# Kernel tuning notes

Hardware: AMD Instinct MI355X
Metric: run time of the kernel (lower is better)

## Reference

```python
import jax, jax.numpy as jnp
import numpy as np

B, H, S, D = 2, 12, 2048, 128
SCALE = D ** (-0.5)
LAMBDA_INIT = 0.8


def setup_inputs() -> dict:
    key = jax.random.key(0)
    ks = jax.random.split(key, 5)
    shp = (B, H, S, D)
    return {
        "q1": jax.random.normal(ks[0], shp, dtype=jnp.float32),
        "k1": jax.random.normal(ks[1], shp, dtype=jnp.float32),
        "v": jax.random.normal(ks[2], shp, dtype=jnp.float32),
        "q2": jax.random.normal(ks[3], shp, dtype=jnp.float32),
        "k2": jax.random.normal(ks[4], shp, dtype=jnp.float32),
        # learnable lambda parameter, stored in log space (lambda_init=0.8)
        "lambda_log": jnp.full((1,), np.log(LAMBDA_INIT), dtype=jnp.float32),
    }


def _causal_attn(q, k, v, causal_mask):
    # q,k,v: [B,H,S,D]; causal_mask: [S,S] bool (True = keep)
    scores = jnp.einsum("bhqd,bhkd->bhqk", q, k) * SCALE
    neg = jnp.asarray(jnp.finfo(scores.dtype).min, scores.dtype)
    scores = jnp.where(causal_mask, scores, neg)
    weights = jax.nn.softmax(scores, axis=-1)
    return jnp.einsum("bhqk,bhkd->bhqd", weights, v)


def reference(q1, k1, v, q2, k2, lambda_log):
    seq = q1.shape[2]
    causal_mask = jnp.tril(jnp.ones((seq, seq), dtype=bool))
    attn1 = _causal_attn(q1, k1, v, causal_mask)
    attn2 = _causal_attn(q2, k2, v, causal_mask)
    lambda_val = jnp.exp(lambda_log).astype(q1.dtype)  # scalar-shaped (1,)
    return attn1 - lambda_val * attn2
```

## Files before the change

kernel.cpp:

```cpp
#include <hip/hip_runtime.h>

#define S_LEN 2048
#define D_DIM 128
#define NBH   24
#define TELEM (NBH * S_LEN * D_DIM)
#define SC2  (0.08838834764831845f * 1.44269504088896f)
#define MFIX 20.0f

typedef __bf16 bf16x8 __attribute__((ext_vector_type(8)));
typedef float f32x4 __attribute__((ext_vector_type(4)));
union Frag { bf16x8 v; unsigned short h[8]; uint4 q; };

#define PSTR 40
#define BUFU 12288
#define SMEM_USH (2 * BUFU)

__device__ __forceinline__ unsigned short f2bf(float f) {
    union { float f; unsigned u; } x; x.f = f;
    unsigned r = x.u + 0x7fffu + ((x.u >> 16) & 1u);
    return (unsigned short)(r >> 16);
}
__device__ __forceinline__ unsigned pk2bf(float a, float b) {
    return (unsigned)f2bf(a) | ((unsigned)f2bf(b) << 16);
}

typedef __attribute__((address_space(1))) const unsigned int gu32;
typedef __attribute__((address_space(3))) unsigned int lu32;
__device__ __forceinline__ void g2l16(const unsigned short* g, unsigned short* l) {
    __builtin_amdgcn_global_load_lds((gu32*)g, (lu32*)l, 16, 0, 0);
}

#define KBLK (TELEM / (8 * 256))
__global__ __launch_bounds__(256) void conv_kv(
    const float* __restrict__ gk1, const float* __restrict__ gk2, const float* __restrict__ gv,
    unsigned short* __restrict__ ok1, unsigned short* __restrict__ ok2,
    unsigned short* __restrict__ ovt)
{
    __shared__ __align__(16) unsigned short sT[128 * 40];
    const int b = blockIdx.x;
    if (b < 2 * KBLK) {
        const float* src = (b < KBLK) ? gk1 : gk2;
        unsigned short* dst = (b < KBLK) ? ok1 : ok2;
        const int bb = (b < KBLK) ? b : b - KBLK;
        const size_t base = ((size_t)bb * 256 + threadIdx.x) * 8;
        float4 a = *(const float4*)(src + base);
        float4 c = *(const float4*)(src + base + 4);
        uint4 w = {pk2bf(a.x, a.y), pk2bf(a.z, a.w), pk2bf(c.x, c.y), pk2bf(c.z, c.w)};
        *(uint4*)(dst + base) = w;
        return;
    }
    const int bx  = b - 2 * KBLK;
    const int tid  = threadIdx.x;
    const int wave = tid >> 6;
    const int lane = tid & 63;
    const int quad = lane >> 4;
    const int l16  = lane & 15;
    const int bh = bx >> 6;
    const int s0 = (bx & 63) * 32;
    const float* pv = gv + (size_t)bh * S_LEN * D_DIM + (size_t)s0 * D_DIM;
    const int vd0 = (wave >> 1) * 64 + l16 * 4;
    const int pq  = ((quad & 1) << 1) | (quad >> 1);
    #pragma unroll
    for (int i = 0; i < 4; ++i) {
        const int kvb = i * 8 + (wave & 1) * 4;
        float4 f = *(const float4*)(pv + (kvb + quad) * D_DIM + vd0);
        unsigned h01 = pk2bf(f.x, f.y), h23 = pk2bf(f.z, f.w);
        unsigned t01 = (unsigned)__shfl_xor((int)h01, 16);
        unsigned t23 = (unsigned)__shfl_xor((int)h23, 16);
        unsigned b01, b23;
        if (quad & 1) {
            b01 = (t23 & 0xffffu) | (h23 << 16);
            b23 = (t23 >> 16) | (h23 & 0xffff0000u);
        } else {
            b01 = (h01 & 0xffffu) | (t01 << 16);
            b23 = (h01 >> 16) | (t01 & 0xffff0000u);
        }
        unsigned s01 = (unsigned)__shfl_xor((int)b01, 32);
        unsigned s23 = (unsigned)__shfl_xor((int)b23, 32);
        uint2 w;
        if (quad & 2) { w.x = s23; w.y = b23; }
        else          { w.x = b01; w.y = s01; }
        *(uint2*)&sT[(vd0 + pq) * 40 + kvb] = w;
    }
    __syncthreads();
    const int d = tid >> 1;
    const int h = tid & 1;
    uint4 w0 = *(const uint4*)&sT[d * 40 + h * 16];
    uint4 w1 = *(const uint4*)&sT[d * 40 + h * 16 + 8];
    unsigned short* out = ovt + ((size_t)bh * D_DIM + d) * S_LEN + s0 + h * 16;
    *(uint4*)(out) = w0;
    *(uint4*)(out + 8) = w1;
}

__device__ __forceinline__ void stage_tile(
    unsigned short* smem, int boff, int w,
    const int* koff, const int* voff,
    const unsigned short* k1pl, const unsigned short* k2pl, const unsigned short* vpl,
    int kv0)
{
    const unsigned short* kp1 = k1pl + (size_t)kv0 * 128;
    const unsigned short* kp2 = k2pl + (size_t)kv0 * 128;
    const unsigned short* vp  = vpl + kv0;
    unsigned short* dk1 = smem + boff + w * 1024;
    unsigned short* dk2 = smem + boff + 4096 + w * 1024;
    unsigned short* dv  = smem + boff + 8192 + w * 1024;
    #pragma unroll
    for (int j = 0; j < 2; ++j) {
        g2l16(kp1 + koff[j], dk1 + j * 512);
        g2l16(kp2 + koff[j], dk2 + j * 512);
        g2l16(vp  + voff[j], dv  + j * 512);
    }
}

__global__ __launch_bounds__(256, 3) void diff_attn_fast(
    const float* __restrict__ gq1, const float* __restrict__ gq2,
    const float* __restrict__ gll,
    const unsigned short* __restrict__ k1b, const unsigned short* __restrict__ k2b,
    const unsigned short* __restrict__ vtb, float* __restrict__ gout)
{
    __shared__ __align__(16) unsigned short smem[SMEM_USH];

    const int tid  = threadIdx.x;
    const int w    = tid >> 6;
    const int lane = tid & 63;
    const int quad = lane >> 4;
    const int l16  = lane & 15;
    const int g    = w & 1;

    const int bid   = blockIdx.x;
    const int pairi = bid / NBH;
    const int bh    = bid - pairi * NBH;
    const int qw    = (w < 2) ? pairi * 32 : (63 - pairi) * 32;
    const int s_idx = qw >> 5;
    const int mytiles = s_idx + 1;
    const int T     = 64 - pairi;
    const size_t hoff = (size_t)bh * (S_LEN * D_DIM);

    const float lam = __expf(gll[0]);

    Frag q1f[4], q2f[4];
    {
        const float* p1 = gq1 + hoff + (size_t)(qw + g * 16 + l16) * D_DIM;
        const float* p2 = gq2 + hoff + (size_t)(qw + g * 16 + l16) * D_DIM;
        #pragma unroll
        for (int ks = 0; ks < 4; ++ks) {
            const int d0 = ks * 32 + quad * 8;
            float4 a = *(const float4*)(p1 + d0);
            float4 b = *(const float4*)(p1 + d0 + 4);
            q1f[ks].q = (uint4){pk2bf(a.x, a.y), pk2bf(a.z, a.w),
                                pk2bf(b.x, b.y), pk2bf(b.z, b.w)};
            a = *(const float4*)(p2 + d0);
            b = *(const float4*)(p2 + d0 + 4);
            q2f[ks].q = (uint4){pk2bf(a.x, a.y), pk2bf(a.z, a.w),
                                pk2bf(b.x, b.y), pk2bf(b.z, b.w)};
        }
    }

    int koff[2], voff[2];
    #pragma unroll
    for (int j = 0; j < 2; ++j) {
        const int s = w * 8 + j * 4 + quad;
        koff[j] = s * 128 + ((l16 ^ (s & 15)) << 3);
        const int d = w * 32 + j * 16 + (lane >> 2);
        voff[j] = d * 2048 + (((lane & 3) ^ ((d >> 1) & 3)) << 3);
    }
    const unsigned short* k1pl = k1b + hoff;
    const unsigned short* k2pl = k2b + hoff;
    const unsigned short* vpl  = vtb + hoff;

    f32x4 o1[8], o2[8];
    #pragma unroll
    for (int i = 0; i < 8; ++i) {
        o1[i] = (f32x4){0.f, 0.f, 0.f, 0.f};
        o2[i] = (f32x4){0.f, 0.f, 0.f, 0.f};
    }
    float l1a = 0.f, l2a = 0.f;

    __asm__ __volatile__("s_waitcnt vmcnt(0)" ::: "memory");
    stage_tile(smem, 0, w, koff, voff, k1pl, k2pl, vpl, 0);

    int boff = 0;
    for (int t = 0; t < T; ++t) {
        const int nboff = boff ^ BUFU;
        if (t + 1 < T) {
            stage_tile(smem, nboff, w, koff, voff, k1pl, k2pl, vpl, (t + 1) * 32);
            __asm__ __volatile__("s_waitcnt vmcnt(6)" ::: "memory");
        } else {
            __asm__ __volatile__("s_waitcnt vmcnt(0)" ::: "memory");
        }
        __builtin_amdgcn_s_barrier();
        __asm__ __volatile__("" ::: "memory");

        if (t < mytiles) {
            const unsigned short* sK1 = smem + boff;
            const unsigned short* sK2 = smem + boff + 4096;
            const unsigned short* sVt = smem + boff + 8192;
            const int kv0 = t * 32;

            f32x4 sA[2], sB[2];
            #pragma unroll
            for (int sub = 0; sub < 2; ++sub) {
                sA[sub] = (f32x4){0.f, 0.f, 0.f, 0.f};
                sB[sub] = (f32x4){0.f, 0.f, 0.f, 0.f};
            }
            __builtin_amdgcn_s_setprio(1);
            #pragma unroll
            for (int sub = 0; sub < 2; ++sub) {
                const int srow = (sub * 16 + l16) * 128;
                #pragma unroll
                for (int ks = 0; ks < 4; ++ks) {
                    const int c = ks * 4 + quad;
                    Frag kf;
                    kf.q = *(const uint4*)&sK1[srow + ((c ^ l16) << 3)];
                    sA[sub] = __builtin_amdgcn_mfma_f32_16x16x32_bf16(kf.v, q1f[ks].v, sA[sub], 0, 0, 0);
                    kf.q = *(const uint4*)&sK2[srow + ((c ^ l16) << 3)];
                    sB[sub] = __builtin_amdgcn_mfma_f32_16x16x32_bf16(kf.v, q2f[ks].v, sB[sub], 0, 0, 0);
                }
            }
            __builtin_amdgcn_s_setprio(0);

            const bool full = (t < s_idx);
            float p1v[8], p2v[8];
            if (full) {
                #pragma unroll
                for (int sub = 0; sub < 2; ++sub)
                    #pragma unroll
                    for (int r = 0; r < 4; ++r) {
                        p1v[sub * 4 + r] = __builtin_amdgcn_exp2f(sA[sub][r] * SC2 - MFIX);
                        p2v[sub * 4 + r] = __builtin_amdgcn_exp2f(sB[sub][r] * SC2 - MFIX);
                    }
            } else {
                const int qv = qw + g * 16 + l16;
                #pragma unroll
                for (int sub = 0; sub < 2; ++sub)
                    #pragma unroll
                    for (int r = 0; r < 4; ++r) {
                        const int kv = kv0 + sub * 16 + quad * 4 + r;
                        const bool ok = (kv <= qv);
                        p1v[sub * 4 + r] = __builtin_amdgcn_exp2f(ok ? sA[sub][r] * SC2 - MFIX : -1e30f);
                        p2v[sub * 4 + r] = __builtin_amdgcn_exp2f(ok ? sB[sub][r] * SC2 - MFIX : -1e30f);
                    }
            }
            float a1 = 0.f, a2 = 0.f;
            #pragma unroll
            for (int i = 0; i < 8; ++i) { a1 += p1v[i]; a2 += p2v[i]; }
            l1a += a1; l2a += a2;

            Frag pf1, pf2;
            {
                unsigned a0 = pk2bf(p1v[0], p1v[1]);
                unsigned a1w = pk2bf(p1v[2], p1v[3]);
                unsigned a2 = pk2bf(p1v[4], p1v[5]);
                unsigned a3 = pk2bf(p1v[6], p1v[7]);
                asm("v_permlane32_swap_b32 %0, %1" : "+v"(a0), "+v"(a2));
                asm("v_permlane32_swap_b32 %0, %1" : "+v"(a1w), "+v"(a3));
                asm("v_permlane16_swap_b32 %0, %1" : "+v"(a0), "+v"(a2));
                asm("v_permlane16_swap_b32 %0, %1" : "+v"(a1w), "+v"(a3));
                pf1.q = (uint4){a0, a1w, a2, a3};
                unsigned b0 = pk2bf(p2v[0], p2v[1]);
                unsigned b1w = pk2bf(p2v[2], p2v[3]);
                unsigned b2 = pk2bf(p2v[4], p2v[5]);
                unsigned b3 = pk2bf(p2v[6], p2v[7]);
                asm("v_permlane32_swap_b32 %0, %1" : "+v"(b0), "+v"(b2));
                asm("v_permlane32_swap_b32 %0, %1" : "+v"(b1w), "+v"(b3));
                asm("v_permlane16_swap_b32 %0, %1" : "+v"(b0), "+v"(b2));
                asm("v_permlane16_swap_b32 %0, %1" : "+v"(b1w), "+v"(b3));
                pf2.q = (uint4){b0, b1w, b2, b3};
            }

            __builtin_amdgcn_s_setprio(1);
            #pragma unroll
            for (int cb = 0; cb < 8; ++cb) {
                const int d = cb * 16 + l16;
                Frag vf;
                vf.q = *(const uint4*)&sVt[d * 32 + ((quad ^ ((d >> 1) & 3)) << 3)];
                o1[cb] = __builtin_amdgcn_mfma_f32_16x16x32_bf16(vf.v, pf1.v, o1[cb], 0, 0, 0);
                o2[cb] = __builtin_amdgcn_mfma_f32_16x16x32_bf16(vf.v, pf2.v, o2[cb], 0, 0, 0);
            }
            __builtin_amdgcn_s_setprio(0);
        }

        __asm__ __volatile__("s_waitcnt lgkmcnt(0)" ::: "memory");
        __builtin_amdgcn_s_barrier();
        __asm__ __volatile__("" ::: "memory");
        boff = nboff;
    }

    float l1 = l1a, l2 = l2a;
    l1 += __shfl_xor(l1, 16); l1 += __shfl_xor(l1, 32);
    l2 += __shfl_xor(l2, 16); l2 += __shfl_xor(l2, 32);
    const float inv1 = 1.0f / l1;
    const float inv2 = lam / l2;
    float* sO = (float*)smem + w * 2112;
    #pragma unroll
    for (int cb = 0; cb < 8; ++cb) {
        f32x4 r = o1[cb] * inv1 - o2[cb] * inv2;
        *(f32x4*)&sO[l16 * 132 + cb * 16 + quad * 4] = r;
    }
    __asm__ __volatile__("s_waitcnt lgkmcnt(0)" ::: "memory");
    #pragma unroll
    for (int u = 0; u < 8; ++u) {
        const int row = u * 2 + (lane >> 5);
        const int d4  = lane & 31;
        f32x4 vv = *(const f32x4*)&sO[row * 132 + d4 * 4];
        *(f32x4*)(gout + hoff + (size_t)(qw + g * 16 + row) * D_DIM + d4 * 4) = vv;
    }
}

#define KSTR 136
#define VSTR2 40
#define foK1 0
#define foK2 (32 * KSTR)
#define foVt (2 * 32 * KSTR)
#define foP  (2 * 32 * KSTR + 128 * VSTR2)
#define FSMEM (foP + 4 * 2 * 16 * PSTR)

__global__ __launch_bounds__(256) void diff_attn_slow(
    const float* __restrict__ gq1, const float* __restrict__ gk1,
    const float* __restrict__ gv,  const float* __restrict__ gq2,
    const float* __restrict__ gk2, const float* __restrict__ gll,
    float* __restrict__ gout)
{
    __shared__ __align__(16) unsigned short smem[FSMEM];
    unsigned short* sK1 = smem + foK1;
    unsigned short* sK2 = smem + foK2;
    unsigned short* sVt = smem + foVt;

    const int tid  = threadIdx.x;
    const int wave = tid >> 6;
    const int lane = tid & 63;
    const int quad = lane >> 4;
    const int l16  = lane & 15;
    const int qb   = (int)gridDim.x - 1 - (int)blockIdx.x;
    const int bh   = blockIdx.y;
    const size_t hoff = (size_t)bh * S_LEN * D_DIM;
    const int qbase = qb * 64 + wave * 16;

    unsigned short* sP1 = smem + foP + (wave * 2 + 0) * 16 * PSTR;
    unsigned short* sP2 = smem + foP + (wave * 2 + 1) * 16 * PSTR;

    const float lam = __expf(gll[0]);

    Frag q1f[4], q2f[4];
    {
        const float* p1 = gq1 + hoff + (size_t)(qbase + l16) * D_DIM;
        const float* p2 = gq2 + hoff + (size_t)(qbase + l16) * D_DIM;
        #pragma unroll
        for (int ks = 0; ks < 4; ++ks) {
            const int d0 = ks * 32 + quad * 8;
            float4 a = *(const float4*)(p1 + d0);
            float4 b = *(const float4*)(p1 + d0 + 4);
            q1f[ks].q = (uint4){pk2bf(a.x, a.y), pk2bf(a.z, a.w),
                               pk2bf(b.x, b.y), pk2bf(b.z, b.w)};
            a = *(const float4*)(p2 + d0);
            b = *(const float4*)(p2 + d0 + 4);
            q2f[ks].q = (uint4){pk2bf(a.x, a.y), pk2bf(a.z, a.w),
                               pk2bf(b.x, b.y), pk2bf(b.z, b.w)};
        }
    }

    f32x4 o1[8], o2[8];
    #pragma unroll
    for (int i = 0; i < 8; ++i) {
        o1[i] = (f32x4){0.f, 0.f, 0.f, 0.f};
        o2[i] = (f32x4){0.f, 0.f, 0.f, 0.f};
    }
    float m1 = -1e30f, m2 = -1e30f, l1 = 0.f, l2 = 0.f;

    const int ntiles  = qb * 2 + 2;
    const int mytiles = (qbase + 15) / 32 + 1;

    const int vd0 = (wave >> 1) * 64 + l16 * 4;
    const int pq  = ((quad & 1) << 1) | (quad >> 1);

    for (int t = 0; t < ntiles; ++t) {
        __syncthreads();
        const int kv0 = t * 32;
        {
            const float* pk1 = gk1 + hoff + (size_t)kv0 * D_DIM;
            const float* pk2 = gk2 + hoff + (size_t)kv0 * D_DIM;
            #pragma unroll
            for (int i = 0; i < 4; ++i) {
                const int e   = i * 256 + tid;
                const int row = e >> 5;
                const int c4  = e & 31;
                const int go  = row * D_DIM + c4 * 4;
                float4 f = *(const float4*)(pk1 + go);
                uint2 w; w.x = pk2bf(f.x, f.y); w.y = pk2bf(f.z, f.w);
                *(uint2*)&sK1[row * KSTR + c4 * 4] = w;
                f = *(const float4*)(pk2 + go);
                w.x = pk2bf(f.x, f.y); w.y = pk2bf(f.z, f.w);
                *(uint2*)&sK2[row * KSTR + c4 * 4] = w;
            }
        }
        {
            const float* pv = gv + hoff + (size_t)kv0 * D_DIM;
            #pragma unroll
            for (int i = 0; i < 4; ++i) {
                const int kvb = i * 8 + (wave & 1) * 4;
                float4 f = *(const float4*)(pv + (kvb + quad) * D_DIM + vd0);
                unsigned h01 = pk2bf(f.x, f.y), h23 = pk2bf(f.z, f.w);
                unsigned t01 = (unsigned)__shfl_xor((int)h01, 16);
                unsigned t23 = (unsigned)__shfl_xor((int)h23, 16);
                unsigned b01, b23;
                if (quad & 1) {
                    b01 = (t23 & 0xffffu) | (h23 << 16);
                    b23 = (t23 >> 16) | (h23 & 0xffff0000u);
                } else {
                    b01 = (h01 & 0xffffu) | (t01 << 16);
                    b23 = (h01 >> 16) | (t01 & 0xffff0000u);
                }
                unsigned s01 = (unsigned)__shfl_xor((int)b01, 32);
                unsigned s23 = (unsigned)__shfl_xor((int)b23, 32);
                uint2 w;
                if (quad & 2) { w.x = s23; w.y = b23; }
                else          { w.x = b01; w.y = s01; }
                *(uint2*)&sVt[(vd0 + pq) * VSTR2 + kvb] = w;
            }
        }
        __syncthreads();
        if (t >= mytiles) continue;

        f32x4 s1[2], s2[2];
        #pragma unroll
        for (int sub = 0; sub < 2; ++sub) {
            s1[sub] = (f32x4){0.f, 0.f, 0.f, 0.f};
            s2[sub] = (f32x4){0.f, 0.f, 0.f, 0.f};
            const int ro = (sub * 16 + l16) * KSTR + quad * 8;
            #pragma unroll
            for (int ks = 0; ks < 4; ++ks) {
                Frag kf;
                kf.q = *(const uint4*)&sK1[ro + ks * 32];
                s1[sub] = __builtin_amdgcn_mfma_f32_16x16x32_bf16(kf.v, q1f[ks].v, s1[sub], 0, 0, 0);
                kf.q = *(const uint4*)&sK2[ro + ks * 32];
                s2[sub] = __builtin_amdgcn_mfma_f32_16x16x32_bf16(kf.v, q2f[ks].v, s2[sub], 0, 0, 0);
            }
        }

        const int qv = qbase + l16;
        {
            float a[8];
            #pragma unroll
            for (int sub = 0; sub < 2; ++sub)
                #pragma unroll
                for (int r = 0; r < 4; ++r) {
                    const int kv = kv0 + sub * 16 + quad * 4 + r;
                    a[sub * 4 + r] = (kv <= qv) ? s1[sub][r] * SC2 : -__builtin_inff();
                }
            float mt = a[0];
            #pragma unroll
            for (int i = 1; i < 8; ++i) mt = fmaxf(mt, a[i]);
            mt = fmaxf(mt, __shfl_xor(mt, 16));
            mt = fmaxf(mt, __shfl_xor(mt, 32));
            const float mn = fmaxf(m1, mt);
            const float al = __builtin_amdgcn_exp2f(m1 - mn);
            m1 = mn;
            float p[8], rs = 0.f;
            #pragma unroll
            for (int i = 0; i < 8; ++i) { p[i] = __builtin_amdgcn_exp2f(a[i] - mn); rs += p[i]; }
            rs += __shfl_xor(rs, 16);
            rs += __shfl_xor(rs, 32);
            l1 = l1 * al + rs;
            #pragma unroll
            for (int cb = 0; cb < 8; ++cb) o1[cb] *= al;
            uint2 w;
            w.x = pk2bf(p[0], p[1]); w.y = pk2bf(p[2], p[3]);
            *(uint2*)&sP1[l16 * PSTR + quad * 4] = w;
            w.x = pk2bf(p[4], p[5]); w.y = pk2bf(p[6], p[7]);
            *(uint2*)&sP1[l16 * PSTR + 16 + quad * 4] = w;
        }
        {
            float a[8];
            #pragma unroll
            for (int sub = 0; sub < 2; ++sub)
                #pragma unroll
                for (int r = 0; r < 4; ++r) {
                    const int kv = kv0 + sub * 16 + quad * 4 + r;
                    a[sub * 4 + r] = (kv <= qv) ? s2[sub][r] * SC2 : -__builtin_inff();
                }
            float mt = a[0];
            #pragma unroll
            for (int i = 1; i < 8; ++i) mt = fmaxf(mt, a[i]);
            mt = fmaxf(mt, __shfl_xor(mt, 16));
            mt = fmaxf(mt, __shfl_xor(mt, 32));
            const float mn = fmaxf(m2, mt);
            const float al = __builtin_amdgcn_exp2f(m2 - mn);
            m2 = mn;
            float p[8], rs = 0.f;
            #pragma unroll
            for (int i = 0; i < 8; ++i) { p[i] = __builtin_amdgcn_exp2f(a[i] - mn); rs += p[i]; }
            rs += __shfl_xor(rs, 16);
            rs += __shfl_xor(rs, 32);
            l2 = l2 * al + rs;
            #pragma unroll
            for (int cb = 0; cb < 8; ++cb) o2[cb] *= al;
            uint2 w;
            w.x = pk2bf(p[0], p[1]); w.y = pk2bf(p[2], p[3]);
            *(uint2*)&sP2[l16 * PSTR + quad * 4] = w;
            w.x = pk2bf(p[4], p[5]); w.y = pk2bf(p[6], p[7]);
            *(uint2*)&sP2[l16 * PSTR + 16 + quad * 4] = w;
        }

        __asm__ __volatile__("s_waitcnt lgkmcnt(0)" ::: "memory");

        Frag pf1, pf2;
        pf1.q = *(const uint4*)&sP1[l16 * PSTR + quad * 8];
        pf2.q = *(const uint4*)&sP2[l16 * PSTR + quad * 8];
        #pragma unroll
        for (int cb = 0; cb < 8; ++cb) {
            Frag vf;
            vf.q = *(const uint4*)&sVt[(cb * 16 + l16) * VSTR2 + quad * 8];
            o1[cb] = __builtin_amdgcn_mfma_f32_16x16x32_bf16(vf.v, pf1.v, o1[cb], 0, 0, 0);
            o2[cb] = __builtin_amdgcn_mfma_f32_16x16x32_bf16(vf.v, pf2.v, o2[cb], 0, 0, 0);
        }
    }

    __syncthreads();
    float* sO = (float*)smem + wave * (16 * 132);
    const float inv1 = 1.0f / l1;
    const float inv2 = lam / l2;
    #pragma unroll
    for (int cb = 0; cb < 8; ++cb) {
        f32x4 r = o1[cb] * inv1 - o2[cb] * inv2;
        *(f32x4*)&sO[l16 * 132 + cb * 16 + quad * 4] = r;
    }
    __asm__ __volatile__("s_waitcnt lgkmcnt(0)" ::: "memory");
    #pragma unroll
    for (int u = 0; u < 8; ++u) {
        const int row = u * 2 + (lane >> 5);
        const int d4  = lane & 31;
        f32x4 vv = *(const f32x4*)&sO[row * 132 + d4 * 4];
        *(f32x4*)(gout + hoff + (size_t)(qbase + row) * D_DIM + d4 * 4) = vv;
    }
}

extern "C" void kernel_launch(void* const* d_in, const int* in_sizes, int n_in,
                              void* d_out, int out_size, void* d_ws, size_t ws_size,
                              hipStream_t stream) {
    (void)in_sizes; (void)n_in; (void)out_size;
    const float* gq1 = (const float*)d_in[0];
    const float* gk1 = (const float*)d_in[1];
    const float* gv  = (const float*)d_in[2];
    const float* gq2 = (const float*)d_in[3];
    const float* gk2 = (const float*)d_in[4];
    const float* gll = (const float*)d_in[5];
    float* gout = (float*)d_out;

    const size_t need = (size_t)3 * TELEM * sizeof(unsigned short);
    if (ws_size >= need) {
        unsigned short* k1b = (unsigned short*)d_ws;
        unsigned short* k2b = k1b + TELEM;
        unsigned short* vtb = k2b + TELEM;
        hipLaunchKernelGGL(conv_kv, dim3(2 * KBLK + NBH * (S_LEN / 32)), dim3(256), 0, stream,
                           gk1, gk2, gv, k1b, k2b, vtb);
        hipLaunchKernelGGL(diff_attn_fast, dim3(32 * NBH), dim3(256), 0, stream,
                           gq1, gq2, gll, k1b, k2b, vtb, gout);
    } else {
        hipLaunchKernelGGL(diff_attn_slow, dim3(S_LEN / 64, NBH), dim3(256), 0, stream,
                           gq1, gk1, gv, gq2, gk2, gll, gout);
    }
}
```

Before: 243.5 us.

## Pair adjacent query tiles per block and use one barrier per KV step

Each block now processes two adjacent 32-row query tiles (2i and 2i+1) instead of a mirrored pair (i, 63-i), with the largest blocks scheduled first. Both wave groups in a block now have nearly equal causal work, instead of one group idling for most of the KV loop. The pipeline is also restructured: each iteration waits for all outstanding loads, hits a single barrier, then issues the next tile's prefetch, which removes the second per-iteration barrier. In exchange, work across blocks becomes uneven, so overall balance depends on the scheduler picking up the heavy-first ordering well.

```diff
diff --git a/kernel.cpp b/kernel.cpp
--- a/kernel.cpp
+++ b/kernel.cpp
@@ -128,12 +128,13 @@
     const int g    = w & 1;
 
     const int bid   = blockIdx.x;
-    const int pairi = bid / NBH;
-    const int bh    = bid - pairi * NBH;
-    const int qw    = (w < 2) ? pairi * 32 : (63 - pairi) * 32;
-    const int s_idx = qw >> 5;
-    const int mytiles = s_idx + 1;
-    const int T     = 64 - pairi;
+    const int j     = bid / NBH;
+    const int bh    = bid - j * NBH;
+    const int i     = 31 - j;
+    const int T     = 2 * i + 2;
+    const int sidx  = (w < 2) ? (2 * i + 1) : (2 * i);
+    const int qw    = sidx * 32;
+    const int mytiles = sidx + 1;
     const size_t hoff = (size_t)bh * (S_LEN * D_DIM);
 
     const float lam = __expf(gll[0]);
@@ -158,11 +159,11 @@
 
     int koff[2], voff[2];
     #pragma unroll
-    for (int j = 0; j < 2; ++j) {
-        const int s = w * 8 + j * 4 + quad;
-        koff[j] = s * 128 + ((l16 ^ (s & 15)) << 3);
-        const int d = w * 32 + j * 16 + (lane >> 2);
-        voff[j] = d * 2048 + (((lane & 3) ^ ((d >> 1) & 3)) << 3);
+    for (int jj = 0; jj < 2; ++jj) {
+        const int s = w * 8 + jj * 4 + quad;
+        koff[jj] = s * 128 + ((l16 ^ (s & 15)) << 3);
+        const int d = w * 32 + jj * 16 + (lane >> 2);
+        voff[jj] = d * 2048 + (((lane & 3) ^ ((d >> 1) & 3)) << 3);
     }
     const unsigned short* k1pl = k1b + hoff;
     const unsigned short* k2pl = k2b + hoff;
@@ -170,9 +171,9 @@
 
     f32x4 o1[8], o2[8];
     #pragma unroll
-    for (int i = 0; i < 8; ++i) {
-        o1[i] = (f32x4){0.f, 0.f, 0.f, 0.f};
-        o2[i] = (f32x4){0.f, 0.f, 0.f, 0.f};
+    for (int ii = 0; ii < 8; ++ii) {
+        o1[ii] = (f32x4){0.f, 0.f, 0.f, 0.f};
+        o2[ii] = (f32x4){0.f, 0.f, 0.f, 0.f};
     }
     float l1a = 0.f, l2a = 0.f;
 
@@ -182,14 +183,11 @@
     int boff = 0;
     for (int t = 0; t < T; ++t) {
         const int nboff = boff ^ BUFU;
-        if (t + 1 < T) {
-            stage_tile(smem, nboff, w, koff, voff, k1pl, k2pl, vpl, (t + 1) * 32);
-            __asm__ __volatile__("s_waitcnt vmcnt(6)" ::: "memory");
-        } else {
-            __asm__ __volatile__("s_waitcnt vmcnt(0)" ::: "memory");
-        }
+        __asm__ __volatile__("s_waitcnt vmcnt(0) lgkmcnt(0)" ::: "memory");
         __builtin_amdgcn_s_barrier();
         __asm__ __volatile__("" ::: "memory");
+        if (t + 1 < T)
+            stage_tile(smem, nboff, w, koff, voff, k1pl, k2pl, vpl, (t + 1) * 32);
 
         if (t < mytiles) {
             const unsigned short* sK1 = smem + boff;
@@ -219,7 +217,7 @@
             }
             __builtin_amdgcn_s_setprio(0);
 
-            const bool full = (t < s_idx);
+            const bool full = (t < sidx);
             float p1v[8], p2v[8];
             if (full) {
                 #pragma unroll
@@ -243,7 +241,7 @@
             }
             float a1 = 0.f, a2 = 0.f;
             #pragma unroll
-            for (int i = 0; i < 8; ++i) { a1 += p1v[i]; a2 += p2v[i]; }
+            for (int ii = 0; ii < 8; ++ii) { a1 += p1v[ii]; a2 += p2v[ii]; }
             l1a += a1; l2a += a2;
 
             Frag pf1, pf2;
@@ -279,12 +277,12 @@
             }
             __builtin_amdgcn_s_setprio(0);
         }
-
-        __asm__ __volatile__("s_waitcnt lgkmcnt(0)" ::: "memory");
-        __builtin_amdgcn_s_barrier();
-        __asm__ __volatile__("" ::: "memory");
         boff = nboff;
     }
+
+    __asm__ __volatile__("s_waitcnt lgkmcnt(0)" ::: "memory");
+    __builtin_amdgcn_s_barrier();
+    __asm__ __volatile__("" ::: "memory");
 
     float l1 = l1a, l2 = l2a;
     l1 += __shfl_xor(l1, 16); l1 += __shfl_xor(l1, 32);
```

Result: faster. 237.1 us (-2.6%).
